# Optimization experiments

Measured on AMD Instinct MI355X. Metric: run time of the kernel, lower is better.

## Reference

```python
import jax, jax.numpy as jnp
import numpy as np

B, T, E, H = 8, 2048, 1024, 64

def setup_inputs() -> dict:
    key = jax.random.key(0)
    k1, k2, k3, k4 = jax.random.split(key, 4)
    x = jax.random.normal(k1, (B, T, E), dtype=jnp.float32)
    # Linear(E, H, bias=False) weights stored as [E, H] (x @ W)
    s = 1.0 / np.sqrt(E)
    Wk = jax.random.normal(k2, (E, H), dtype=jnp.float32) * s
    Wq = jax.random.normal(k3, (E, H), dtype=jnp.float32) * s
    Wv = jax.random.normal(k4, (E, H), dtype=jnp.float32) * s
    return {"x": x, "Wk": Wk, "Wq": Wq, "Wv": Wv}

def reference(x, Wk, Wq, Wv):
    _, t, e = x.shape
    k = jnp.einsum('bte,eh->bth', x, Wk)
    q = jnp.einsum('bte,eh->bth', x, Wq)
    v = jnp.einsum('bte,eh->bth', x, Wv)
    # NOTE: original scales by E**-0.5 (embedding dim), not head_size**-0.5
    wei = jnp.einsum('bqh,bkh->bqk', q, k) * (e ** -0.5)
    causal = jnp.tril(jnp.ones((t, t), dtype=bool))
    wei = jnp.where(causal, wei, -jnp.inf)
    wei = jax.nn.softmax(wei, axis=-1)
    out = jnp.einsum('bqk,bkh->bqh', wei, v)
    return out
```

## Files before the change

kernel.cpp:

```cpp
#include <hip/hip_runtime.h>

typedef unsigned short u16;
typedef unsigned int u32;
typedef __bf16 bf16x8 __attribute__((ext_vector_type(8)));
typedef __bf16 bf16x4 __attribute__((ext_vector_type(4)));
typedef float f32x4 __attribute__((ext_vector_type(4)));

constexpr int Bn = 8, Tn = 2048, En = 1024, Hn = 64;
constexpr int Mrows = Bn * Tn;
constexpr float CEXP = 0.03125f * 1.4426950408889634f;

__device__ __forceinline__ u16 f2bf(float f) {
  u32 u = __float_as_uint(f);
  return (u16)((u + 0x7fffu + ((u >> 16) & 1u)) >> 16);
}

__global__ __launch_bounds__(256) void wt_kernel(
    const float* __restrict__ Wk, const float* __restrict__ Wq,
    const float* __restrict__ Wv, u16* __restrict__ Wt2) {
  __shared__ float tile[64][68];
  const int mat = blockIdx.x >> 4;
  const int tk = blockIdx.x & 15;
  const float* W = (mat == 0) ? Wk : (mat == 1) ? Wq : Wv;
  const int t = threadIdx.x;
#pragma unroll
  for (int i = 0; i < 4; ++i) {
    const int f = t + i * 256;
    const int el = f >> 4;
    const int h4 = f & 15;
    float4 v = *(const float4*)(W + (size_t)(tk * 64 + el) * Hn + h4 * 4);
    tile[el][h4 * 4 + 0] = v.x;
    tile[el][h4 * 4 + 1] = v.y;
    tile[el][h4 * 4 + 2] = v.z;
    tile[el][h4 * 4 + 3] = v.w;
  }
  __syncthreads();
#pragma unroll
  for (int c2 = 0; c2 < 2; ++c2) {
    const int c = t * 2 + c2;
    const int fi = c >> 6;
    const int l = c & 63;
    const int ht = fi >> 1, kss = fi & 1;
    const int q = l >> 4, l16 = l & 15;
    __align__(16) u16 buf[8];
#pragma unroll
    for (int j = 0; j < 8; ++j)
      buf[j] = f2bf(tile[kss * 32 + q * 8 + j][ht * 16 + l16]);
    u16* dst = Wt2 + ((size_t)(tk * 12 + mat * 4 + ht) * 2 + kss) * 512 + l * 8;
    *(uint4*)dst = *(const uint4*)buf;
  }
}

__global__ __launch_bounds__(256, 2) void qkv_kernel(
    const float* __restrict__ x, const u16* __restrict__ Wt2,
    u16* __restrict__ Kb16, u16* __restrict__ Qb16, u16* __restrict__ Vt16) {
  constexpr int NR = 32, BK = 128, LDK = BK + 8;
  __shared__ u16 xs[NR * LDK];
  const int t = threadIdx.x;
  const int w = t >> 6, lane = t & 63;
  const int quad = lane >> 4, l16 = lane & 15;
  const int r0 = blockIdx.x * NR;

  const int srow = t >> 5;
  const int scol = (t & 31) * 4;
  const float* xp = x + (size_t)(r0 + srow) * En + scol;
  u16* xsw0 = xs + srow * LDK + scol;

  const u16* wA = Wt2 + (size_t)lane * 8;

  f32x4 acc[3][2];
#pragma unroll
  for (int i = 0; i < 3; ++i)
#pragma unroll
    for (int nt = 0; nt < 2; ++nt) acc[i][nt] = (f32x4){0.f, 0.f, 0.f, 0.f};

  bf16x8 af[2][12];

#define LOADA(P, K0)                                                            \
  do {                                                                          \
    const int tb_ = ((K0) >> 6) * 12;                                           \
    _Pragma("unroll") for (int ks_ = 0; ks_ < 4; ++ks_)                         \
        _Pragma("unroll") for (int i_ = 0; i_ < 3; ++i_) {                      \
      const int frag_ = (tb_ + (ks_ >> 1) * 12 + (3 * w + i_)) * 2 + (ks_ & 1); \
      af[P][ks_ * 3 + i_] = *(const bf16x8*)(wA + (size_t)frag_ * 512);         \
    }                                                                           \
  } while (0)

  float4 pre[4];
#pragma unroll
  for (int i = 0; i < 4; ++i) pre[i] = *(const float4*)(xp + i * 8 * En);
  LOADA(0, 0);

#pragma unroll
  for (int s = 0; s < 8; ++s) {
    const int k0 = s * BK;
    const int par = s & 1;
    __syncthreads();
#pragma unroll
    for (int i = 0; i < 4; ++i) {
      bf16x4 pk;
      pk[0] = (__bf16)pre[i].x; pk[1] = (__bf16)pre[i].y;
      pk[2] = (__bf16)pre[i].z; pk[3] = (__bf16)pre[i].w;
      *(bf16x4*)(xsw0 + i * 8 * LDK) = pk;
    }
    __syncthreads();
    if (s < 7) {
#pragma unroll
      for (int i = 0; i < 4; ++i)
        pre[i] = *(const float4*)(xp + k0 + BK + i * 8 * En);
      LOADA(par ^ 1, k0 + BK);
    }
#pragma unroll
    for (int ks = 0; ks < 4; ++ks) {
      bf16x8 b0 = *(const bf16x8*)(xs + l16 * LDK + ks * 32 + quad * 8);
      bf16x8 b1 = *(const bf16x8*)(xs + (16 + l16) * LDK + ks * 32 + quad * 8);
#pragma unroll
      for (int i = 0; i < 3; ++i) {
        acc[i][0] = __builtin_amdgcn_mfma_f32_16x16x32_bf16(af[par][ks * 3 + i], b0, acc[i][0], 0, 0, 0);
        acc[i][1] = __builtin_amdgcn_mfma_f32_16x16x32_bf16(af[par][ks * 3 + i], b1, acc[i][1], 0, 0, 0);
      }
    }
  }
#undef LOADA

#pragma unroll
  for (int i = 0; i < 3; ++i) {
    const int mt = 3 * w + i;
    const int mat = mt >> 2, ht = mt & 3;
#pragma unroll
    for (int nt = 0; nt < 2; ++nt) {
      const int row = r0 + nt * 16 + l16;
      f32x4 a = acc[i][nt];
      if (mat < 2) {
        u16* dst = ((mat == 0) ? Kb16 : Qb16) + (size_t)row * Hn + ht * 16 + quad * 4;
        uint2 pk;
        pk.x = (u32)f2bf(a[0]) | ((u32)f2bf(a[1]) << 16);
        pk.y = (u32)f2bf(a[2]) | ((u32)f2bf(a[3]) << 16);
        *(uint2*)dst = pk;
      } else {
        const int bb = row >> 11, tt = row & 2047;
        u16* base = Vt16 + ((size_t)bb * 64) * Tn + tt;
#pragma unroll
        for (int r = 0; r < 4; ++r)
          base[(size_t)(ht * 16 + quad * 4 + r) * Tn] = f2bf(a[r]);
      }
    }
  }
}

__global__ __launch_bounds__(512, 4) void attn_kernel(
    const u16* __restrict__ Qb16, const u16* __restrict__ Kb16,
    const u16* __restrict__ Vt16, float* __restrict__ out) {
  __shared__ __align__(16) char arena[34816];
  __shared__ float l_sh[8][32];

  u16* ptb = (u16*)arena;
  float* osb = (float*)arena;

  const int idx = blockIdx.x;
  const int b = idx & 7;
  const int tq = 63 - (idx >> 3);
  const int w = threadIdx.x >> 6, lane = threadIdx.x & 63;
  const int quad = lane >> 4, l16 = lane & 15;
  const int qbase = tq * 32;
  const int limit = qbase + 32;
  const int ch = ((limit + 255) >> 8) << 5;
  const int lo = w * ch;
  const int hi = min(lo + ch, limit);
  const int qa_abs = qbase + l16;
  const int qb_abs = qbase + 16 + l16;

  const u16* Kp = Kb16 + (size_t)b * Tn * Hn;
  const u16* Vp = Vt16 + (size_t)b * 64 * Tn;

  const u16* qrowA = Qb16 + ((size_t)b * Tn + qa_abs) * Hn + quad * 8;
  const u16* qrowB = qrowA + (size_t)16 * Hn;
  const bf16x8 qa0 = *(const bf16x8*)(qrowA);
  const bf16x8 qa1 = *(const bf16x8*)(qrowA + 32);
  const bf16x8 qb0 = *(const bf16x8*)(qrowB);
  const bf16x8 qb1 = *(const bf16x8*)(qrowB + 32);

  u16* ptw = ptb + (size_t)w * (2 * 16 * 40);

  f32x4 oA0 = {0.f, 0.f, 0.f, 0.f}, oA1 = oA0, oA2 = oA0, oA3 = oA0;
  f32x4 oB0 = oA0, oB1 = oA0, oB2 = oA0, oB3 = oA0;
  f32x4 laccA = oA0, laccB = oA0;

#pragma unroll 2
  for (int kb = lo; kb < hi; kb += 32) {
    const u16* krow0 = Kp + (size_t)(kb + l16) * Hn + quad * 8;
    const u16* krow1 = krow0 + (size_t)16 * Hn;
    const bf16x8 k0lo = *(const bf16x8*)(krow0);
    const bf16x8 k0hi = *(const bf16x8*)(krow0 + 32);
    const bf16x8 k1lo = *(const bf16x8*)(krow1);
    const bf16x8 k1hi = *(const bf16x8*)(krow1 + 32);

    const f32x4 z = {0.f, 0.f, 0.f, 0.f};
    f32x4 s0a = __builtin_amdgcn_mfma_f32_16x16x32_bf16(k0lo, qa0, z, 0, 0, 0);
    s0a = __builtin_amdgcn_mfma_f32_16x16x32_bf16(k0hi, qa1, s0a, 0, 0, 0);
    f32x4 s1a = __builtin_amdgcn_mfma_f32_16x16x32_bf16(k1lo, qa0, z, 0, 0, 0);
    s1a = __builtin_amdgcn_mfma_f32_16x16x32_bf16(k1hi, qa1, s1a, 0, 0, 0);
    f32x4 s0b = __builtin_amdgcn_mfma_f32_16x16x32_bf16(k0lo, qb0, z, 0, 0, 0);
    s0b = __builtin_amdgcn_mfma_f32_16x16x32_bf16(k0hi, qb1, s0b, 0, 0, 0);
    f32x4 s1b = __builtin_amdgcn_mfma_f32_16x16x32_bf16(k1lo, qb0, z, 0, 0, 0);
    s1b = __builtin_amdgcn_mfma_f32_16x16x32_bf16(k1hi, qb1, s1b, 0, 0, 0);

    if (kb + 15 > qbase) {
#pragma unroll
      for (int r = 0; r < 4; ++r)
        if (kb + quad * 4 + r > qa_abs) s0a[r] = -3.0e38f;
    }
    if (kb + 31 > qbase) {
#pragma unroll
      for (int r = 0; r < 4; ++r)
        if (kb + 16 + quad * 4 + r > qa_abs) s1a[r] = -3.0e38f;
    }
    if (kb + 15 > qbase + 16) {
#pragma unroll
      for (int r = 0; r < 4; ++r)
        if (kb + quad * 4 + r > qb_abs) s0b[r] = -3.0e38f;
    }
    if (kb + 31 > qbase + 16) {
#pragma unroll
      for (int r = 0; r < 4; ++r)
        if (kb + 16 + quad * 4 + r > qb_abs) s1b[r] = -3.0e38f;
    }

    f32x4 pa0, pa1, pb0v, pb1v;
#pragma unroll
    for (int r = 0; r < 4; ++r) {
      pa0[r] = __builtin_amdgcn_exp2f(s0a[r] * CEXP);
      pa1[r] = __builtin_amdgcn_exp2f(s1a[r] * CEXP);
      pb0v[r] = __builtin_amdgcn_exp2f(s0b[r] * CEXP);
      pb1v[r] = __builtin_amdgcn_exp2f(s1b[r] * CEXP);
    }
    laccA += pa0;
    laccA += pa1;
    laccB += pb0v;
    laccB += pb1v;

    {
      bf16x4 wa0, wa1, wb0, wb1;
      wa0[0] = (__bf16)pa0[0]; wa0[1] = (__bf16)pa0[1];
      wa0[2] = (__bf16)pa0[2]; wa0[3] = (__bf16)pa0[3];
      wa1[0] = (__bf16)pa1[0]; wa1[1] = (__bf16)pa1[1];
      wa1[2] = (__bf16)pa1[2]; wa1[3] = (__bf16)pa1[3];
      wb0[0] = (__bf16)pb0v[0]; wb0[1] = (__bf16)pb0v[1];
      wb0[2] = (__bf16)pb0v[2]; wb0[3] = (__bf16)pb0v[3];
      wb1[0] = (__bf16)pb1v[0]; wb1[1] = (__bf16)pb1v[1];
      wb1[2] = (__bf16)pb1v[2]; wb1[3] = (__bf16)pb1v[3];
      *(bf16x4*)&ptw[l16 * 40 + quad * 4] = wa0;
      *(bf16x4*)&ptw[l16 * 40 + 16 + quad * 4] = wa1;
      *(bf16x4*)&ptw[640 + l16 * 40 + quad * 4] = wb0;
      *(bf16x4*)&ptw[640 + l16 * 40 + 16 + quad * 4] = wb1;
    }
    const bf16x8 pba = *(const bf16x8*)&ptw[l16 * 40 + quad * 8];
    const bf16x8 pbb = *(const bf16x8*)&ptw[640 + l16 * 40 + quad * 8];

    const u16* vrow = Vp + (size_t)l16 * Tn + kb + quad * 8;
    const bf16x8 v0 = *(const bf16x8*)(vrow);
    const bf16x8 v1 = *(const bf16x8*)(vrow + (size_t)16 * Tn);
    const bf16x8 v2 = *(const bf16x8*)(vrow + (size_t)32 * Tn);
    const bf16x8 v3 = *(const bf16x8*)(vrow + (size_t)48 * Tn);

    oA0 = __builtin_amdgcn_mfma_f32_16x16x32_bf16(v0, pba, oA0, 0, 0, 0);
    oA1 = __builtin_amdgcn_mfma_f32_16x16x32_bf16(v1, pba, oA1, 0, 0, 0);
    oA2 = __builtin_amdgcn_mfma_f32_16x16x32_bf16(v2, pba, oA2, 0, 0, 0);
    oA3 = __builtin_amdgcn_mfma_f32_16x16x32_bf16(v3, pba, oA3, 0, 0, 0);
    oB0 = __builtin_amdgcn_mfma_f32_16x16x32_bf16(v0, pbb, oB0, 0, 0, 0);
    oB1 = __builtin_amdgcn_mfma_f32_16x16x32_bf16(v1, pbb, oB1, 0, 0, 0);
    oB2 = __builtin_amdgcn_mfma_f32_16x16x32_bf16(v2, pbb, oB2, 0, 0, 0);
    oB3 = __builtin_amdgcn_mfma_f32_16x16x32_bf16(v3, pbb, oB3, 0, 0, 0);
  }

  float la = (laccA[0] + laccA[1]) + (laccA[2] + laccA[3]);
  la += __shfl_xor(la, 16);
  la += __shfl_xor(la, 32);
  float lb = (laccB[0] + laccB[1]) + (laccB[2] + laccB[3]);
  lb += __shfl_xor(lb, 16);
  lb += __shfl_xor(lb, 32);
  if (quad == 0) {
    l_sh[w][l16] = la;
    l_sh[w][16 + l16] = lb;
  }
  __syncthreads();

  if (w < 4) {
    float* o0 = osb + ((size_t)w * 32 + l16) * 68;
    *(f32x4*)(o0 + 0 * 16 + quad * 4) = oA0;
    *(f32x4*)(o0 + 1 * 16 + quad * 4) = oA1;
    *(f32x4*)(o0 + 2 * 16 + quad * 4) = oA2;
    *(f32x4*)(o0 + 3 * 16 + quad * 4) = oA3;
    float* o1 = osb + ((size_t)w * 32 + 16 + l16) * 68;
    *(f32x4*)(o1 + 0 * 16 + quad * 4) = oB0;
    *(f32x4*)(o1 + 1 * 16 + quad * 4) = oB1;
    *(f32x4*)(o1 + 2 * 16 + quad * 4) = oB2;
    *(f32x4*)(o1 + 3 * 16 + quad * 4) = oB3;
  }
  __syncthreads();

  const int qq = threadIdx.x >> 4, dq = threadIdx.x & 15;
  f32x4 part = {0.f, 0.f, 0.f, 0.f};
#pragma unroll
  for (int ww = 0; ww < 4; ++ww)
    part += *(const f32x4*)&osb[((size_t)ww * 32 + qq) * 68 + dq * 4];
  __syncthreads();

  if (w >= 4) {
    float* o0 = osb + ((size_t)(w - 4) * 32 + l16) * 68;
    *(f32x4*)(o0 + 0 * 16 + quad * 4) = oA0;
    *(f32x4*)(o0 + 1 * 16 + quad * 4) = oA1;
    *(f32x4*)(o0 + 2 * 16 + quad * 4) = oA2;
    *(f32x4*)(o0 + 3 * 16 + quad * 4) = oA3;
    float* o1 = osb + ((size_t)(w - 4) * 32 + 16 + l16) * 68;
    *(f32x4*)(o1 + 0 * 16 + quad * 4) = oB0;
    *(f32x4*)(o1 + 1 * 16 + quad * 4) = oB1;
    *(f32x4*)(o1 + 2 * 16 + quad * 4) = oB2;
    *(f32x4*)(o1 + 3 * 16 + quad * 4) = oB3;
  }
  __syncthreads();

#pragma unroll
  for (int ww = 0; ww < 4; ++ww)
    part += *(const f32x4*)&osb[((size_t)ww * 32 + qq) * 68 + dq * 4];

  float lg = 0.f;
#pragma unroll
  for (int ww = 0; ww < 8; ++ww) lg += l_sh[ww][qq];
  part *= (1.f / lg);
  *(f32x4*)(out + ((size_t)b * Tn + qbase + qq) * Hn + dq * 4) = part;
}

extern "C" void kernel_launch(void* const* d_in, const int* in_sizes, int n_in,
                              void* d_out, int out_size, void* d_ws, size_t ws_size,
                              hipStream_t stream) {
  const void* x = nullptr;
  const void* Ws[3] = {nullptr, nullptr, nullptr};
  int wj = 0;
  for (int i = 0; i < n_in; ++i) {
    if (in_sizes[i] == Bn * Tn * En) x = d_in[i];
    else if (wj < 3) Ws[wj++] = d_in[i];
  }
  const float* Wk = (const float*)Ws[0];
  const float* Wq = (const float*)Ws[1];
  const float* Wv = (const float*)Ws[2];

  u16* Kb16 = (u16*)d_ws;
  u16* Qb16 = Kb16 + (size_t)Mrows * Hn;
  u16* Vt16 = Qb16 + (size_t)Mrows * Hn;
  u16* Wt2  = Vt16 + (size_t)Mrows * Hn;

  wt_kernel<<<48, 256, 0, stream>>>(Wk, Wq, Wv, Wt2);
  qkv_kernel<<<Mrows / 32, 256, 0, stream>>>((const float*)x, Wt2, Kb16, Qb16, Vt16);
  attn_kernel<<<Bn * (Tn / 32), 512, 0, stream>>>(Qb16, Kb16, Vt16, (float*)d_out);
}
```

Baseline: 134.8 us.

## Double the QKV projection row tile and double-buffer the x tile in LDS

The QKV projection kernel now processes 64 rows per block instead of 32, so each weight fragment loaded into registers feeds twice as many MFMAs. The x staging tile is double-buffered in LDS, which removes one barrier per K step and lets the conversion and store of the next tile overlap the current step's MFMAs. Each thread now loads 32 contiguous floats per row. The cost is more registers (launch bounds drop to one block per SM), twice the LDS, and half as many blocks.

Measured after the change: 135.8 us. Within noise of the previous version (+0.7%).

```diff
diff --git a/kernel.cpp b/kernel.cpp
--- a/kernel.cpp
+++ b/kernel.cpp
@@ -51,30 +51,36 @@
   }
 }
 
-__global__ __launch_bounds__(256, 2) void qkv_kernel(
+__global__ __launch_bounds__(256, 1) void qkv_kernel(
     const float* __restrict__ x, const u16* __restrict__ Wt2,
     u16* __restrict__ Kb16, u16* __restrict__ Qb16, u16* __restrict__ Vt16) {
-  constexpr int NR = 32, BK = 128, LDK = BK + 8;
-  __shared__ u16 xs[NR * LDK];
+  constexpr int NR = 64, BK = 128, LDK = BK + 8;
+  __shared__ u16 xs[2][NR * LDK];
   const int t = threadIdx.x;
   const int w = t >> 6, lane = t & 63;
   const int quad = lane >> 4, l16 = lane & 15;
   const int r0 = blockIdx.x * NR;
 
-  const int srow = t >> 5;
-  const int scol = (t & 31) * 4;
+  const int srow = t >> 2;
+  const int scol = (t & 3) * 32;
   const float* xp = x + (size_t)(r0 + srow) * En + scol;
-  u16* xsw0 = xs + srow * LDK + scol;
 
   const u16* wA = Wt2 + (size_t)lane * 8;
 
-  f32x4 acc[3][2];
+  f32x4 acc[3][4];
 #pragma unroll
   for (int i = 0; i < 3; ++i)
 #pragma unroll
-    for (int nt = 0; nt < 2; ++nt) acc[i][nt] = (f32x4){0.f, 0.f, 0.f, 0.f};
+    for (int rt = 0; rt < 4; ++rt) acc[i][rt] = (f32x4){0.f, 0.f, 0.f, 0.f};
 
   bf16x8 af[2][12];
+  float4 pre[8];
+
+#define LOADP(K0)                                                    \
+  do {                                                               \
+    _Pragma("unroll") for (int j_ = 0; j_ < 8; ++j_)                 \
+        pre[j_] = *(const float4*)(xp + (K0) + j_ * 4);              \
+  } while (0)
 
 #define LOADA(P, K0)                                                            \
   do {                                                                          \
@@ -86,51 +92,57 @@
     }                                                                           \
   } while (0)
 
-  float4 pre[4];
-#pragma unroll
-  for (int i = 0; i < 4; ++i) pre[i] = *(const float4*)(xp + i * 8 * En);
+#define WRITEX(B)                                                    \
+  do {                                                               \
+    u16* d_ = &xs[B][srow * LDK + scol];                             \
+    _Pragma("unroll") for (int j_ = 0; j_ < 4; ++j_) {               \
+      bf16x8 pk_;                                                    \
+      pk_[0] = (__bf16)pre[2 * j_].x;  pk_[1] = (__bf16)pre[2 * j_].y;  \
+      pk_[2] = (__bf16)pre[2 * j_].z;  pk_[3] = (__bf16)pre[2 * j_].w;  \
+      pk_[4] = (__bf16)pre[2 * j_ + 1].x; pk_[5] = (__bf16)pre[2 * j_ + 1].y; \
+      pk_[6] = (__bf16)pre[2 * j_ + 1].z; pk_[7] = (__bf16)pre[2 * j_ + 1].w; \
+      *(bf16x8*)(d_ + j_ * 8) = pk_;                                 \
+    }                                                                \
+  } while (0)
+
+  LOADP(0);
   LOADA(0, 0);
+  WRITEX(0);
+  LOADP(BK);
 
 #pragma unroll
   for (int s = 0; s < 8; ++s) {
-    const int k0 = s * BK;
-    const int par = s & 1;
-    __syncthreads();
-#pragma unroll
-    for (int i = 0; i < 4; ++i) {
-      bf16x4 pk;
-      pk[0] = (__bf16)pre[i].x; pk[1] = (__bf16)pre[i].y;
-      pk[2] = (__bf16)pre[i].z; pk[3] = (__bf16)pre[i].w;
-      *(bf16x4*)(xsw0 + i * 8 * LDK) = pk;
-    }
     __syncthreads();
     if (s < 7) {
-#pragma unroll
-      for (int i = 0; i < 4; ++i)
-        pre[i] = *(const float4*)(xp + k0 + BK + i * 8 * En);
-      LOADA(par ^ 1, k0 + BK);
-    }
+      WRITEX((s + 1) & 1);
+      if (s < 6) LOADP((s + 2) * BK);
+      LOADA((s + 1) & 1, (s + 1) * BK);
+    }
+    const u16* xb = &xs[s & 1][0];
 #pragma unroll
     for (int ks = 0; ks < 4; ++ks) {
-      bf16x8 b0 = *(const bf16x8*)(xs + l16 * LDK + ks * 32 + quad * 8);
-      bf16x8 b1 = *(const bf16x8*)(xs + (16 + l16) * LDK + ks * 32 + quad * 8);
-#pragma unroll
-      for (int i = 0; i < 3; ++i) {
-        acc[i][0] = __builtin_amdgcn_mfma_f32_16x16x32_bf16(af[par][ks * 3 + i], b0, acc[i][0], 0, 0, 0);
-        acc[i][1] = __builtin_amdgcn_mfma_f32_16x16x32_bf16(af[par][ks * 3 + i], b1, acc[i][1], 0, 0, 0);
+#pragma unroll
+      for (int rt = 0; rt < 4; ++rt) {
+        bf16x8 b = *(const bf16x8*)(xb + (rt * 16 + l16) * LDK + ks * 32 + quad * 8);
+#pragma unroll
+        for (int i = 0; i < 3; ++i)
+          acc[i][rt] = __builtin_amdgcn_mfma_f32_16x16x32_bf16(af[s & 1][ks * 3 + i], b,
+                                                               acc[i][rt], 0, 0, 0);
       }
     }
   }
+#undef LOADP
 #undef LOADA
+#undef WRITEX
 
 #pragma unroll
   for (int i = 0; i < 3; ++i) {
     const int mt = 3 * w + i;
     const int mat = mt >> 2, ht = mt & 3;
 #pragma unroll
-    for (int nt = 0; nt < 2; ++nt) {
-      const int row = r0 + nt * 16 + l16;
-      f32x4 a = acc[i][nt];
+    for (int rt = 0; rt < 4; ++rt) {
+      const int row = r0 + rt * 16 + l16;
+      f32x4 a = acc[i][rt];
       if (mat < 2) {
         u16* dst = ((mat == 0) ? Kb16 : Qb16) + (size_t)row * Hn + ht * 16 + quad * 4;
         uint2 pk;
@@ -351,6 +363,6 @@
   u16* Wt2  = Vt16 + (size_t)Mrows * Hn;
 
   wt_kernel<<<48, 256, 0, stream>>>(Wk, Wq, Wv, Wt2);
-  qkv_kernel<<<Mrows / 32, 256, 0, stream>>>((const float*)x, Wt2, Kb16, Qb16, Vt16);
+  qkv_kernel<<<Mrows / 64, 256, 0, stream>>>((const float*)x, Wt2, Kb16, Qb16, Vt16);
   attn_kernel<<<Bn * (Tn / 32), 512, 0, stream>>>(Qb16, Kb16, Vt16, (float*)d_out);
 }
```
